# Kernel optimization log

Measured on AMD Instinct MI355X. Metric: run time of the kernel, lower is better.

Reference implementation:

```python
import jax, jax.numpy as jnp
import numpy as np

Z_SIZE, KEY_SIZE, HID = 128, 256, 512
NEG = -1e9


def setup_inputs() -> dict:
    key = jax.random.key(0)
    ks = jax.random.split(key, 8)
    B, T, H, W, Y = 512, 32, 32, 32, 4
    D = H * W
    g = lambda k, shape, s: jax.random.normal(k, shape, jnp.float32) * s
    return {
        "x_seq": jax.random.normal(ks[0], (B, T, H, W), jnp.float32),
        # Encoder (conv encoder stand-in: flatten -> MLP -> z_size)
        "enc_w1": g(ks[1], (D, HID), 0.03),
        "enc_b1": jnp.zeros((HID,), jnp.float32),
        "enc_w2": g(ks[2], (HID, Z_SIZE), 0.05),
        "enc_b2": jnp.zeros((Z_SIZE,), jnp.float32),
        # LSTM input kernel (recurrent kernel unused: h_prev is always 0)
        "lstm_Wx": g(ks[3], (KEY_SIZE + 1, 4 * HID), 0.05),
        "lstm_b": jnp.zeros((4 * HID,), jnp.float32),
        "keyw_W": g(ks[4], (HID, KEY_SIZE), 0.05),
        "keyw_b": jnp.zeros((KEY_SIZE,), jnp.float32),
        "g_W": g(ks[5], (HID, 1), 0.05),
        "g_b": jnp.zeros((1,), jnp.float32),
        "y_W": g(ks[6], (HID, Y), 0.05),
        "y_b": jnp.zeros((Y,), jnp.float32),
        "conf_gain": jnp.float32(1.0),
        "conf_bias": jnp.float32(0.0),
    }


def reference(x_seq, enc_w1, enc_b1, enc_w2, enc_b2, lstm_Wx, lstm_b,
              keyw_W, keyw_b, g_W, g_b, y_W, y_b, conf_gain, conf_bias):
    B, T = x_seq.shape[0], x_seq.shape[1]
    Y = y_b.shape[0]
    dt = x_seq.dtype

    # Encode all frames at once: (B, T, Z)
    x_flat = x_seq.reshape(B, T, -1)
    z_seq = jax.nn.relu(x_flat @ enc_w1 + enc_b1) @ enc_w2 + enc_b2
    # Pad with the zero z_t used at the final step t == T  -> (B, T+1, Z)
    z_pad = jnp.concatenate([z_seq, jnp.zeros((B, 1, Z_SIZE), dt)], axis=1)

    def lstm_step(x):  # single keras LSTM step from zero state (h=c=0)
        gates = x @ lstm_Wx + lstm_b
        i, f, c, o = jnp.split(gates, 4, axis=-1)  # keras gate order i,f,c,o
        c_new = jax.nn.sigmoid(i) * jnp.tanh(c)     # f*c_prev = 0
        return jax.nn.sigmoid(o) * jnp.tanh(c_new)

    slot_idx = jnp.arange(T + 1)

    def step(carry, t):
        key_r, M_k, M_v, _ = carry
        z_t = z_pad[:, t]                       # (B, Z)
        h = lstm_step(key_r)                    # (B, HID)
        key_w = h @ keyw_W + keyw_b             # (B, KEY)
        gate = jax.nn.sigmoid(h @ g_W + g_b)    # (B, 1)
        y_lin = h @ y_W + y_b                   # (B, Y)

        # Content-based read over memory slots written so far (slots < t)
        scores = jnp.einsum('bz,btz->bt', z_t, M_v)          # (B, T+1)
        valid = (slot_idx < t)[None, :]
        w_k = jax.nn.softmax(jnp.where(valid, scores, NEG), axis=1)
        c_k = jax.nn.sigmoid(scores * conf_gain + conf_bias)  # (B, T+1)
        Mkc = jnp.concatenate([M_k, c_k[..., None]], axis=-1)  # (B, T+1, KEY+1)
        key_r_new = gate * jnp.einsum('bt,btk->bk', w_k, Mkc)
        key_r_new = jnp.where(t == 0, jnp.zeros_like(key_r_new), key_r_new)

        # Memory write (append == write into preallocated slot t)
        M_k = M_k.at[:, t].set(key_w)
        M_v = M_v.at[:, t].set(z_t)
        return (key_r_new, M_k, M_v, y_lin), None

    init = (jnp.zeros((B, KEY_SIZE + 1), dt),
            jnp.zeros((B, T + 1, KEY_SIZE), dt),
            jnp.zeros((B, T + 1, Z_SIZE), dt),
            jnp.zeros((B, Y), dt))
    (_, _, _, y_pred_linear), _ = jax.lax.scan(step, init, jnp.arange(T + 1))
    y_pred = jnp.argmax(y_pred_linear, axis=1)
    return y_pred_linear, y_pred
```

## Files before the change

kernel.cpp:

```cpp
#include <hip/hip_runtime.h>
#include <math.h>

__device__ __forceinline__ float sigf(float x) { return 1.0f / (1.0f + expf(-x)); }
__device__ __forceinline__ float4 f4fma(float s, float4 b, float4 a) {
  return make_float4(fmaf(s, b.x, a.x), fmaf(s, b.y, a.y), fmaf(s, b.z, a.z), fmaf(s, b.w, a.w));
}
__device__ __forceinline__ void wave_red16_32(float4& v) {
  v.x += __shfl_xor(v.x, 16); v.y += __shfl_xor(v.y, 16);
  v.z += __shfl_xor(v.z, 16); v.w += __shfl_xor(v.w, 16);
  v.x += __shfl_xor(v.x, 32); v.y += __shfl_xor(v.y, 32);
  v.z += __shfl_xor(v.z, 32); v.w += __shfl_xor(v.w, 32);
}
__device__ __forceinline__ void wave_red8_16_32(float4& v) {
  v.x += __shfl_xor(v.x, 8);  v.y += __shfl_xor(v.y, 8);
  v.z += __shfl_xor(v.z, 8);  v.w += __shfl_xor(v.w, 8);
  wave_red16_32(v);
}

__global__ __launch_bounds__(256) void k_gemm1(const float* __restrict__ X,
                                               const float* __restrict__ W,
                                               const float* __restrict__ Bv,
                                               float* __restrict__ C)
{
  const int K = 1024, N = 512;
  __shared__ float As[32][68];
  __shared__ float Bs[32][132];
  const int tid = threadIdx.x;
  const int bm = blockIdx.x >> 2;
  const int bn = blockIdx.x & 3;
  const int ty = tid >> 4, tx = tid & 15;
  const int ar = tid & 63, ac4 = (tid >> 6) * 4;
  const int wk = tid >> 3, wc = (tid & 7) * 16;
  const float* Xb = X + (size_t)(bm * 64 + ar) * K;
  const float* Wb = W + bn * 128 + wc;
  float acc[4][8];
#pragma unroll
  for (int i = 0; i < 4; i++)
#pragma unroll
    for (int j = 0; j < 8; j++) acc[i][j] = 0.f;

  float4 pa0, pa1, pw0, pw1, pw2, pw3;
  {
    pa0 = *(const float4*)(Xb + ac4);
    pa1 = *(const float4*)(Xb + ac4 + 16);
    const float* wr = Wb + (size_t)wk * N;
    pw0 = *(const float4*)(wr);
    pw1 = *(const float4*)(wr + 4);
    pw2 = *(const float4*)(wr + 8);
    pw3 = *(const float4*)(wr + 12);
  }
  for (int k0 = 0; k0 < K; k0 += 32) {
    if (k0) __syncthreads();
    As[ac4 + 0][ar] = pa0.x; As[ac4 + 1][ar] = pa0.y;
    As[ac4 + 2][ar] = pa0.z; As[ac4 + 3][ar] = pa0.w;
    As[ac4 + 16][ar] = pa1.x; As[ac4 + 17][ar] = pa1.y;
    As[ac4 + 18][ar] = pa1.z; As[ac4 + 19][ar] = pa1.w;
    *(float4*)(&Bs[wk][wc])      = pw0;
    *(float4*)(&Bs[wk][wc + 4])  = pw1;
    *(float4*)(&Bs[wk][wc + 8])  = pw2;
    *(float4*)(&Bs[wk][wc + 12]) = pw3;
    __syncthreads();
    if (k0 < K - 32) {
      const int kn = k0 + 32;
      pa0 = *(const float4*)(Xb + kn + ac4);
      pa1 = *(const float4*)(Xb + kn + ac4 + 16);
      const float* wr = Wb + (size_t)(kn + wk) * N;
      pw0 = *(const float4*)(wr);
      pw1 = *(const float4*)(wr + 4);
      pw2 = *(const float4*)(wr + 8);
      pw3 = *(const float4*)(wr + 12);
    }
#pragma unroll
    for (int kk = 0; kk < 32; kk++) {
      float4 a = *(const float4*)(&As[kk][ty * 4]);
      float4 bA = *(const float4*)(&Bs[kk][tx * 4]);
      float4 bB = *(const float4*)(&Bs[kk][64 + tx * 4]);
      float ar4[4] = {a.x, a.y, a.z, a.w};
#pragma unroll
      for (int i = 0; i < 4; i++) {
        acc[i][0] = fmaf(ar4[i], bA.x, acc[i][0]);
        acc[i][1] = fmaf(ar4[i], bA.y, acc[i][1]);
        acc[i][2] = fmaf(ar4[i], bA.z, acc[i][2]);
        acc[i][3] = fmaf(ar4[i], bA.w, acc[i][3]);
        acc[i][4] = fmaf(ar4[i], bB.x, acc[i][4]);
        acc[i][5] = fmaf(ar4[i], bB.y, acc[i][5]);
        acc[i][6] = fmaf(ar4[i], bB.z, acc[i][6]);
        acc[i][7] = fmaf(ar4[i], bB.w, acc[i][7]);
      }
    }
  }
  const int crow0 = bm * 64 + ty * 4;
  const int ccolA = bn * 128 + tx * 4;
  const int ccolB = ccolA + 64;
  float4 bvA = *(const float4*)(Bv + ccolA);
  float4 bvB = *(const float4*)(Bv + ccolB);
#pragma unroll
  for (int i = 0; i < 4; i++) {
    float4 vA = make_float4(acc[i][0] + bvA.x, acc[i][1] + bvA.y,
                            acc[i][2] + bvA.z, acc[i][3] + bvA.w);
    float4 vB = make_float4(acc[i][4] + bvB.x, acc[i][5] + bvB.y,
                            acc[i][6] + bvB.z, acc[i][7] + bvB.w);
    vA.x = fmaxf(vA.x, 0.f); vA.y = fmaxf(vA.y, 0.f);
    vA.z = fmaxf(vA.z, 0.f); vA.w = fmaxf(vA.w, 0.f);
    vB.x = fmaxf(vB.x, 0.f); vB.y = fmaxf(vB.y, 0.f);
    vB.z = fmaxf(vB.z, 0.f); vB.w = fmaxf(vB.w, 0.f);
    *(float4*)(&C[(size_t)(crow0 + i) * N + ccolA]) = vA;
    *(float4*)(&C[(size_t)(crow0 + i) * N + ccolB]) = vB;
  }
}

__global__ __launch_bounds__(256) void k_gemm2(const float* __restrict__ A,
                                               const float* __restrict__ W,
                                               const float* __restrict__ Bv,
                                               float* __restrict__ zp)
{
  const int K = 512, N = 128;
  __shared__ float As[16][36];
  __shared__ float Bs[16][132];
  const int tid = threadIdx.x;
  const int bm = blockIdx.x;
  const int ty = tid >> 4, tx = tid & 15;
  const int ar = tid & 31, ac4 = ((tid >> 5) & 3) * 4;
  const int bk = tid >> 4, bc8 = (tid & 15) * 8;
  float acc[2][8];
#pragma unroll
  for (int i = 0; i < 2; i++)
#pragma unroll
    for (int j = 0; j < 8; j++) acc[i][j] = 0.f;

  for (int k0 = 0; k0 < K; k0 += 16) {
    if (tid < 128) {
      float4 av = *(const float4*)(A + (size_t)(bm * 32 + ar) * K + k0 + ac4);
      As[ac4 + 0][ar] = av.x; As[ac4 + 1][ar] = av.y;
      As[ac4 + 2][ar] = av.z; As[ac4 + 3][ar] = av.w;
    }
    *(float4*)(&Bs[bk][bc8]) = *(const float4*)(W + (size_t)(k0 + bk) * N + bc8);
    *(float4*)(&Bs[bk][bc8 + 4]) = *(const float4*)(W + (size_t)(k0 + bk) * N + bc8 + 4);
    __syncthreads();
#pragma unroll
    for (int kk = 0; kk < 16; kk++) {
      float a0 = As[kk][ty * 2], a1 = As[kk][ty * 2 + 1];
      float4 bA = *(const float4*)(&Bs[kk][tx * 4]);
      float4 bB = *(const float4*)(&Bs[kk][64 + tx * 4]);
      acc[0][0] = fmaf(a0, bA.x, acc[0][0]); acc[0][1] = fmaf(a0, bA.y, acc[0][1]);
      acc[0][2] = fmaf(a0, bA.z, acc[0][2]); acc[0][3] = fmaf(a0, bA.w, acc[0][3]);
      acc[0][4] = fmaf(a0, bB.x, acc[0][4]); acc[0][5] = fmaf(a0, bB.y, acc[0][5]);
      acc[0][6] = fmaf(a0, bB.z, acc[0][6]); acc[0][7] = fmaf(a0, bB.w, acc[0][7]);
      acc[1][0] = fmaf(a1, bA.x, acc[1][0]); acc[1][1] = fmaf(a1, bA.y, acc[1][1]);
      acc[1][2] = fmaf(a1, bA.z, acc[1][2]); acc[1][3] = fmaf(a1, bA.w, acc[1][3]);
      acc[1][4] = fmaf(a1, bB.x, acc[1][4]); acc[1][5] = fmaf(a1, bB.y, acc[1][5]);
      acc[1][6] = fmaf(a1, bB.z, acc[1][6]); acc[1][7] = fmaf(a1, bB.w, acc[1][7]);
    }
    __syncthreads();
  }
  const int ccolA = tx * 4, ccolB = ccolA + 64;
  float4 bvA = *(const float4*)(Bv + ccolA);
  float4 bvB = *(const float4*)(Bv + ccolB);
#pragma unroll
  for (int i = 0; i < 2; i++) {
    int r = bm * 32 + ty * 2 + i;
    int b = r >> 5, tt = r & 31;
    float4 vA = make_float4(acc[i][0] + bvA.x, acc[i][1] + bvA.y,
                            acc[i][2] + bvA.z, acc[i][3] + bvA.w);
    float4 vB = make_float4(acc[i][4] + bvB.x, acc[i][5] + bvB.y,
                            acc[i][6] + bvB.z, acc[i][7] + bvB.w);
    *(float4*)(&zp[(size_t)b * 4096 + tt * 128 + ccolA]) = vA;
    *(float4*)(&zp[(size_t)b * 4096 + tt * 128 + ccolB]) = vB;
  }
}

__global__ __launch_bounds__(256) void k_gram(const float* __restrict__ zp,
                                              float* __restrict__ warr,
                                              float* __restrict__ wc,
                                              const float* __restrict__ cgp,
                                              const float* __restrict__ cbp)
{
  __shared__ float zl[32][128];
  __shared__ float sg[32][32];
  int b = blockIdx.x, tid = threadIdx.x;
  const float* zb = zp + (size_t)b * 4096;
  for (int i = tid; i < 32 * 128; i += 256) (&zl[0][0])[i] = zb[i];
  __syncthreads();
  for (int p = tid; p < 496; p += 256) {
    int t = 1;
    while (p >= t * (t + 1) / 2) t++;
    int tp = p - t * (t - 1) / 2;
    const float* za = &zl[t][0];
    const float* zc = &zl[tp][0];
    float s = 0.f;
#pragma unroll 4
    for (int c = 0; c < 128; c += 4) {
      s += za[c] * zc[c] + za[c + 1] * zc[c + 1] + za[c + 2] * zc[c + 2] + za[c + 3] * zc[c + 3];
    }
    sg[t][tp] = s;
  }
  __syncthreads();
  if (tid >= 1 && tid < 32) {
    int t = tid;
    float cg = cgp[0], cb = cbp[0];
    float m = -3.0e38f;
    for (int tp = 0; tp < t; tp++) m = fmaxf(m, sg[t][tp]);
    float se = 0.f;
    for (int tp = 0; tp < t; tp++) se += expf(sg[t][tp] - m);
    float inv = 1.0f / se;
    float wcs = 0.f;
    for (int tp = 0; tp < t; tp++) {
      float s = sg[t][tp];
      float w = expf(s - m) * inv;
      warr[(size_t)b * 1024 + t * 32 + tp] = w;
      wcs = fmaf(w, sigf(fmaf(s, cg, cb)), wcs);
    }
    wc[b * 32 + t] = wcs;
  }
}

__global__ __launch_bounds__(256) void k_gates(const float* __restrict__ Wx,
                                               const float* __restrict__ lb,
                                               const float* __restrict__ keyrT,
                                               float* __restrict__ h, int t)
{
  __shared__ float smem[4608];
  float* As = smem;
  float* Bs = smem + 1280;
  float* Rb = smem;
  const int tid = threadIdx.x;
  const int rt = blockIdx.x >> 5;
  const int ct = blockIdx.x & 31;
  const int row0 = rt * 16;
  const int hc0 = ct * 16;

  if (t > 0) {
    const int ksub = tid >> 3;
    const int pos = tid & 7;
    const int rg = pos >> 2;
    const int cg = pos & 3;
    const int kkS = tid >> 2;
    const int lS = (tid & 3) * 4;
    float4 aI[8], aC[8], aO[8];
#pragma unroll
    for (int r = 0; r < 8; r++) {
      aI[r] = make_float4(0.f, 0.f, 0.f, 0.f);
      aC[r] = make_float4(0.f, 0.f, 0.f, 0.f);
      aO[r] = make_float4(0.f, 0.f, 0.f, 0.f);
    }
    float4 pA, pB0, pB1, pB2;
    {
      pA = *(const float4*)&keyrT[(size_t)kkS * 512 + row0 + lS];
      const float* wrow = Wx + (size_t)kkS * 2048 + hc0 + lS;
      pB0 = *(const float4*)(wrow);
      pB1 = *(const float4*)(wrow + 1024);
      pB2 = *(const float4*)(wrow + 1536);
    }
    for (int c = 0; c < 4; ++c) {
      if (c) __syncthreads();
      *(float4*)&As[kkS * 20 + lS] = pA;
      *(float4*)&Bs[kkS * 52 + lS] = pB0;
      *(float4*)&Bs[kkS * 52 + 16 + lS] = pB1;
      *(float4*)&Bs[kkS * 52 + 32 + lS] = pB2;
      __syncthreads();
      if (c < 3) {
        const int kn = (c + 1) * 64 + kkS;
        pA = *(const float4*)&keyrT[(size_t)kn * 512 + row0 + lS];
        const float* wrow = Wx + (size_t)kn * 2048 + hc0 + lS;
        pB0 = *(const float4*)(wrow);
        pB1 = *(const float4*)(wrow + 1024);
        pB2 = *(const float4*)(wrow + 1536);
      }
#pragma unroll
      for (int i = 0; i < 2; ++i) {
        const int kk = ksub * 2 + i;
        float a8[8];
        *(float4*)&a8[0] = *(const float4*)&As[kk * 20 + rg * 8];
        *(float4*)&a8[4] = *(const float4*)&As[kk * 20 + rg * 8 + 4];
        float4 bI = *(const float4*)&Bs[kk * 52 + cg * 4];
        float4 bC = *(const float4*)&Bs[kk * 52 + 16 + cg * 4];
        float4 bO = *(const float4*)&Bs[kk * 52 + 32 + cg * 4];
#pragma unroll
        for (int r = 0; r < 8; r++) {
          float a = a8[r];
          aI[r] = f4fma(a, bI, aI[r]);
          aC[r] = f4fma(a, bC, aC[r]);
          aO[r] = f4fma(a, bO, aO[r]);
        }
      }
    }
    if (tid < 8) {
      float a8[8];
      *(float4*)&a8[0] = *(const float4*)&keyrT[(size_t)256 * 512 + row0 + rg * 8];
      *(float4*)&a8[4] = *(const float4*)&keyrT[(size_t)256 * 512 + row0 + rg * 8 + 4];
      const float* wrow = Wx + (size_t)256 * 2048 + hc0 + cg * 4;
      float4 bI = *(const float4*)(wrow);
      float4 bC = *(const float4*)(wrow + 1024);
      float4 bO = *(const float4*)(wrow + 1536);
#pragma unroll
      for (int r = 0; r < 8; r++) {
        float a = a8[r];
        aI[r] = f4fma(a, bI, aI[r]);
        aC[r] = f4fma(a, bC, aC[r]);
        aO[r] = f4fma(a, bO, aO[r]);
      }
    }
#pragma unroll
    for (int r = 0; r < 8; r++) { wave_red8_16_32(aI[r]); wave_red8_16_32(aC[r]); wave_red8_16_32(aO[r]); }
    __syncthreads();
    {
      const int wave = tid >> 6, lane = tid & 63;
      if (lane < 8) {
        float* w = &Rb[wave * 800 + lane * 100];
#pragma unroll
        for (int r = 0; r < 8; r++) {
          *(float4*)&w[r * 12 + 0] = aI[r];
          *(float4*)&w[r * 12 + 4] = aC[r];
          *(float4*)&w[r * 12 + 8] = aO[r];
        }
      }
    }
    __syncthreads();
    {
      const int r = tid >> 4;
      const int hc = tid & 15;
      const int p = (r >> 3) * 4 + (hc >> 2);
      const int base = p * 100 + (r & 7) * 12 + (hc & 3);
      float sI = Rb[base]     + Rb[800 + base]     + Rb[1600 + base]     + Rb[2400 + base];
      float sC = Rb[base + 4] + Rb[800 + base + 4] + Rb[1600 + base + 4] + Rb[2400 + base + 4];
      float sO = Rb[base + 8] + Rb[800 + base + 8] + Rb[1600 + base + 8] + Rb[2400 + base + 8];
      float iv = sI + lb[hc0 + hc];
      float cv = sC + lb[1024 + hc0 + hc];
      float ov = sO + lb[1536 + hc0 + hc];
      h[(size_t)(row0 + r) * 512 + hc0 + hc] = sigf(ov) * tanhf(sigf(iv) * tanhf(cv));
    }
  } else {
    const int r = tid >> 4;
    const int hc = tid & 15;
    float hv = sigf(lb[1536 + hc0 + hc]) * tanhf(sigf(lb[hc0 + hc]) * tanhf(lb[1024 + hc0 + hc]));
    h[(size_t)(row0 + r) * 512 + hc0 + hc] = hv;
  }
}

__global__ __launch_bounds__(256) void k_update(const float* __restrict__ h,
                                                const float* __restrict__ kW,
                                                const float* __restrict__ kb,
                                                const float* __restrict__ gW,
                                                const float* __restrict__ gb,
                                                const float* __restrict__ warr,
                                                const float* __restrict__ wc,
                                                float* __restrict__ Mk,
                                                float* __restrict__ keyrT, int t)
{
  __shared__ float smem[10640];
  float* hs  = smem;
  float* gWs = smem + 8256;
  float* wws = smem + 8768;
  float* gsh = smem + 9344;
  float* kWs = smem + 9360;
  float* Rb  = smem + 9360;
  const int tid = threadIdx.x;
  const int rt = blockIdx.x >> 4;
  const int ct = blockIdx.x & 15;
  const int row0 = rt * 16;
  const int c0 = ct * 16;

  {
    const int r = tid >> 4, seg = tid & 15;
    const float* hrow = h + (size_t)(row0 + r) * 512 + seg * 32;
    float* hd = hs + r * 516 + seg * 32;
#pragma unroll
    for (int q = 0; q < 8; ++q) {
      const int qp = ((q + seg) & 7) * 4;
      *(float4*)&hd[qp] = *(const float4*)&hrow[qp];
    }
    if (tid < 128) *(float4*)&gWs[tid * 4] = *(const float4*)&gW[tid * 4];
    wws[r * 36 + seg]      = (seg < t)      ? warr[(size_t)(row0 + r) * 1024 + t * 32 + seg] : 0.f;
    wws[r * 36 + 16 + seg] = (16 + seg < t) ? warr[(size_t)(row0 + r) * 1024 + t * 32 + 16 + seg] : 0.f;
  }
  const int kkW = tid >> 2, lW = (tid & 3) * 4;
  float4 pW = *(const float4*)&kW[(size_t)kkW * 256 + c0 + lW];
  __syncthreads();

  const int ksub = tid >> 4, pu = tid & 15, rgu = pu >> 2, cgu = pu & 3;
  float4 au[4];
#pragma unroll
  for (int r = 0; r < 4; r++) au[r] = make_float4(0.f, 0.f, 0.f, 0.f);
  for (int c = 0; c < 8; ++c) {
    if (c) __syncthreads();
    *(float4*)&kWs[kkW * 20 + lW] = pW;
    __syncthreads();
    if (c < 7) pW = *(const float4*)&kW[(size_t)((c + 1) * 64 + kkW) * 256 + c0 + lW];
#pragma unroll
    for (int i = 0; i < 4; ++i) {
      const int kk = ksub * 4 + i;
      float4 b4 = *(const float4*)&kWs[kk * 20 + cgu * 4];
      const int kidx = c * 64 + kk;
#pragma unroll
      for (int jj = 0; jj < 4; ++jj) {
        float a = hs[(rgu * 4 + jj) * 516 + kidx];
        au[jj] = f4fma(a, b4, au[jj]);
      }
    }
  }
#pragma unroll
  for (int r = 0; r < 4; r++) wave_red16_32(au[r]);
  __syncthreads();
  {
    const int wave = tid >> 6, lane = tid & 63;
    if (lane < 16) {
      float* w = &Rb[wave * 320 + lane * 20];
#pragma unroll
      for (int r = 0; r < 4; r++) *(float4*)&w[r * 4] = au[r];
    }
  }
  __syncthreads();
  {
    const int r = tid >> 4, cc = tid & 15;
    const int p = (r >> 2) * 4 + (cc >> 2);
    const int e = p * 20 + (r & 3) * 4 + (cc & 3);
    float v = Rb[e] + Rb[320 + e] + Rb[640 + e] + Rb[960 + e];
    Mk[(size_t)(row0 + r) * 8192 + t * 256 + c0 + cc] = v + kb[c0 + cc];
  }
  {
    const int r = tid >> 4, seg = tid & 15;
    const float* hp = &hs[r * 516 + seg * 32];
    const float* gp = &gWs[seg * 32];
    float s = 0.f;
#pragma unroll 8
    for (int j = 0; j < 32; ++j) s = fmaf(hp[j], gp[j], s);
    s += __shfl_xor(s, 1); s += __shfl_xor(s, 2);
    s += __shfl_xor(s, 4); s += __shfl_xor(s, 8);
    if (seg == 0) gsh[r] = sigf(s + gb[0]);
  }
  __syncthreads();
  {
    const int r = tid >> 4, cc = tid & 15;
    const int row = row0 + r;
    if (t == 0) {
      keyrT[(size_t)(c0 + cc) * 512 + row] = 0.f;
      if (ct == 0 && cc == 0) keyrT[(size_t)256 * 512 + row] = 0.f;
    } else {
      float a = 0.f;
      const float* mkb = Mk + (size_t)row * 8192 + c0 + cc;
      const float* wp = &wws[r * 36];
      for (int tp = 0; tp < t; ++tp) a = fmaf(wp[tp], mkb[tp * 256], a);
      float g = gsh[r];
      keyrT[(size_t)(c0 + cc) * 512 + row] = g * a;
      if (ct == 0 && cc == 0)
        keyrT[(size_t)256 * 512 + row] = g * wc[row * 32 + t];
    }
  }
}

__global__ __launch_bounds__(256) void k_y(const float* __restrict__ h,
                                           const float* __restrict__ yW,
                                           const float* __restrict__ yb,
                                           float* __restrict__ out)
{
  int tid = threadIdx.x;
  int wave = tid >> 6, lane = tid & 63;
  int row = blockIdx.x * 4 + wave;
  float a0 = 0.f, a1 = 0.f, a2 = 0.f, a3 = 0.f;
  for (int k = lane; k < 512; k += 64) {
    float hv = h[(size_t)row * 512 + k];
    float4 w4 = *(const float4*)(yW + k * 4);
    a0 = fmaf(hv, w4.x, a0);
    a1 = fmaf(hv, w4.y, a1);
    a2 = fmaf(hv, w4.z, a2);
    a3 = fmaf(hv, w4.w, a3);
  }
#pragma unroll
  for (int off = 32; off > 0; off >>= 1) {
    a0 += __shfl_xor(a0, off);
    a1 += __shfl_xor(a1, off);
    a2 += __shfl_xor(a2, off);
    a3 += __shfl_xor(a3, off);
  }
  if (lane == 0) {
    a0 += yb[0]; a1 += yb[1]; a2 += yb[2]; a3 += yb[3];
    out[row * 4 + 0] = a0;
    out[row * 4 + 1] = a1;
    out[row * 4 + 2] = a2;
    out[row * 4 + 3] = a3;
    int bi = 0; float bv = a0;
    if (a1 > bv) { bv = a1; bi = 1; }
    if (a2 > bv) { bv = a2; bi = 2; }
    if (a3 > bv) { bv = a3; bi = 3; }
    out[2048 + row] = (float)bi;
  }
}

extern "C" void kernel_launch(void* const* d_in, const int* in_sizes, int n_in,
                              void* d_out, int out_size, void* d_ws, size_t ws_size,
                              hipStream_t stream)
{
  const float* x  = (const float*)d_in[0];
  const float* w1 = (const float*)d_in[1];
  const float* b1 = (const float*)d_in[2];
  const float* w2 = (const float*)d_in[3];
  const float* b2 = (const float*)d_in[4];
  const float* Wx = (const float*)d_in[5];
  const float* lb = (const float*)d_in[6];
  const float* kW = (const float*)d_in[7];
  const float* kb = (const float*)d_in[8];
  const float* gW = (const float*)d_in[9];
  const float* gb = (const float*)d_in[10];
  const float* yW = (const float*)d_in[11];
  const float* yb = (const float*)d_in[12];
  const float* cg = (const float*)d_in[13];
  const float* cb = (const float*)d_in[14];
  float* out = (float*)d_out;
  char* ws = (char*)d_ws;
  float* C1    = (float*)(ws);
  float* Mk    = (float*)(ws);
  float* warr  = (float*)(ws + 16777216);
  float* wcb   = (float*)(ws + 18874368);
  float* keyrT = (float*)(ws + 18939904);
  float* h     = (float*)(ws + 19466240);
  float* zp    = (float*)(ws + 33554432);

  hipLaunchKernelGGL(k_gemm1, dim3(1024), dim3(256), 0, stream, x, w1, b1, C1);
  hipLaunchKernelGGL(k_gemm2, dim3(512), dim3(256), 0, stream, C1, w2, b2, zp);
  hipLaunchKernelGGL(k_gram, dim3(512), dim3(256), 0, stream, zp, warr, wcb, cg, cb);
  for (int t = 0; t <= 32; t++) {
    hipLaunchKernelGGL(k_gates, dim3(1024), dim3(256), 0, stream, Wx, lb, keyrT, h, t);
    if (t < 32) {
      hipLaunchKernelGGL(k_update, dim3(512), dim3(256), 0, stream,
                         h, kW, kb, gW, gb, warr, wcb, Mk, keyrT, t);
    }
  }
  hipLaunchKernelGGL(k_y, dim3(128), dim3(256), 0, stream, h, yW, yb, out);
}
```

Baseline: 1.431 ms.

## Simplify gemm1, gates and update kernels to naive per-thread dot products

The gemm1 kernel drops its register-prefetch double buffering and halves the K tile to 16, adding a second barrier per tile. The gates kernel moves from a split-K register-tiled GEMM with shuffle reductions to one where each thread computes two hidden columns for one row, reading the weights directly from global memory. Its grid shrinks to 512 blocks. The update kernel likewise replaces its tiled shared-memory GEMM with a per-thread 512-long dot product reading keyW from global memory. This gives simpler code and fewer syncs and reductions, at the cost of less data reuse, less latency hiding and more global traffic.

After: 2.499 ms. 1.75x slower.

```diff
diff --git a/kernel.cpp b/kernel.cpp
--- a/kernel.cpp
+++ b/kernel.cpp
@@ -2,20 +2,6 @@
 #include <math.h>
 
 __device__ __forceinline__ float sigf(float x) { return 1.0f / (1.0f + expf(-x)); }
-__device__ __forceinline__ float4 f4fma(float s, float4 b, float4 a) {
-  return make_float4(fmaf(s, b.x, a.x), fmaf(s, b.y, a.y), fmaf(s, b.z, a.z), fmaf(s, b.w, a.w));
-}
-__device__ __forceinline__ void wave_red16_32(float4& v) {
-  v.x += __shfl_xor(v.x, 16); v.y += __shfl_xor(v.y, 16);
-  v.z += __shfl_xor(v.z, 16); v.w += __shfl_xor(v.w, 16);
-  v.x += __shfl_xor(v.x, 32); v.y += __shfl_xor(v.y, 32);
-  v.z += __shfl_xor(v.z, 32); v.w += __shfl_xor(v.w, 32);
-}
-__device__ __forceinline__ void wave_red8_16_32(float4& v) {
-  v.x += __shfl_xor(v.x, 8);  v.y += __shfl_xor(v.y, 8);
-  v.z += __shfl_xor(v.z, 8);  v.w += __shfl_xor(v.w, 8);
-  wave_red16_32(v);
-}
 
 __global__ __launch_bounds__(256) void k_gemm1(const float* __restrict__ X,
                                                const float* __restrict__ W,
@@ -23,55 +9,32 @@
                                                float* __restrict__ C)
 {
   const int K = 1024, N = 512;
-  __shared__ float As[32][68];
-  __shared__ float Bs[32][132];
+  __shared__ float As[16][68];
+  __shared__ float Bs[16][132];
   const int tid = threadIdx.x;
   const int bm = blockIdx.x >> 2;
   const int bn = blockIdx.x & 3;
   const int ty = tid >> 4, tx = tid & 15;
   const int ar = tid & 63, ac4 = (tid >> 6) * 4;
-  const int wk = tid >> 3, wc = (tid & 7) * 16;
+  const int bk = tid >> 4, bc8 = (tid & 15) * 8;
   const float* Xb = X + (size_t)(bm * 64 + ar) * K;
-  const float* Wb = W + bn * 128 + wc;
   float acc[4][8];
 #pragma unroll
   for (int i = 0; i < 4; i++)
 #pragma unroll
     for (int j = 0; j < 8; j++) acc[i][j] = 0.f;
 
-  float4 pa0, pa1, pw0, pw1, pw2, pw3;
-  {
-    pa0 = *(const float4*)(Xb + ac4);
-    pa1 = *(const float4*)(Xb + ac4 + 16);
-    const float* wr = Wb + (size_t)wk * N;
-    pw0 = *(const float4*)(wr);
-    pw1 = *(const float4*)(wr + 4);
-    pw2 = *(const float4*)(wr + 8);
-    pw3 = *(const float4*)(wr + 12);
-  }
-  for (int k0 = 0; k0 < K; k0 += 32) {
-    if (k0) __syncthreads();
-    As[ac4 + 0][ar] = pa0.x; As[ac4 + 1][ar] = pa0.y;
-    As[ac4 + 2][ar] = pa0.z; As[ac4 + 3][ar] = pa0.w;
-    As[ac4 + 16][ar] = pa1.x; As[ac4 + 17][ar] = pa1.y;
-    As[ac4 + 18][ar] = pa1.z; As[ac4 + 19][ar] = pa1.w;
-    *(float4*)(&Bs[wk][wc])      = pw0;
-    *(float4*)(&Bs[wk][wc + 4])  = pw1;
-    *(float4*)(&Bs[wk][wc + 8])  = pw2;
-    *(float4*)(&Bs[wk][wc + 12]) = pw3;
-    __syncthreads();
-    if (k0 < K - 32) {
-      const int kn = k0 + 32;
-      pa0 = *(const float4*)(Xb + kn + ac4);
-      pa1 = *(const float4*)(Xb + kn + ac4 + 16);
-      const float* wr = Wb + (size_t)(kn + wk) * N;
-      pw0 = *(const float4*)(wr);
-      pw1 = *(const float4*)(wr + 4);
-      pw2 = *(const float4*)(wr + 8);
-      pw3 = *(const float4*)(wr + 12);
-    }
-#pragma unroll
-    for (int kk = 0; kk < 32; kk++) {
+  for (int k0 = 0; k0 < K; k0 += 16) {
+    float4 av = *(const float4*)(Xb + k0 + ac4);
+    float4 b0 = *(const float4*)(W + (size_t)(k0 + bk) * N + bn * 128 + bc8);
+    float4 b1 = *(const float4*)(W + (size_t)(k0 + bk) * N + bn * 128 + bc8 + 4);
+    As[ac4 + 0][ar] = av.x; As[ac4 + 1][ar] = av.y;
+    As[ac4 + 2][ar] = av.z; As[ac4 + 3][ar] = av.w;
+    *(float4*)(&Bs[bk][bc8]) = b0;
+    *(float4*)(&Bs[bk][bc8 + 4]) = b1;
+    __syncthreads();
+#pragma unroll
+    for (int kk = 0; kk < 16; kk++) {
       float4 a = *(const float4*)(&As[kk][ty * 4]);
       float4 bA = *(const float4*)(&Bs[kk][tx * 4]);
       float4 bB = *(const float4*)(&Bs[kk][64 + tx * 4]);
@@ -88,6 +51,7 @@
         acc[i][7] = fmaf(ar4[i], bB.w, acc[i][7]);
       }
     }
+    __syncthreads();
   }
   const int crow0 = bm * 64 + ty * 4;
   const int ccolA = bn * 128 + tx * 4;
@@ -219,122 +183,57 @@
                                                const float* __restrict__ keyrT,
                                                float* __restrict__ h, int t)
 {
-  __shared__ float smem[4608];
-  float* As = smem;
-  float* Bs = smem + 1280;
-  float* Rb = smem;
+  __shared__ float As[257 * 17 + 3];
   const int tid = threadIdx.x;
-  const int rt = blockIdx.x >> 5;
-  const int ct = blockIdx.x & 31;
+  const int rt = blockIdx.x >> 4;
+  const int ct = blockIdx.x & 15;
   const int row0 = rt * 16;
-  const int hc0 = ct * 16;
+  const int hc0 = ct * 32;
+  const int r = tid >> 4;
+  const int c2 = tid & 15;
+  const int j0 = hc0 + c2 * 2;
+
+  float aI0 = lb[j0],        aI1 = lb[j0 + 1];
+  float aC0 = lb[1024 + j0], aC1 = lb[1024 + j0 + 1];
+  float aO0 = lb[1536 + j0], aO1 = lb[1536 + j0 + 1];
 
   if (t > 0) {
-    const int ksub = tid >> 3;
-    const int pos = tid & 7;
-    const int rg = pos >> 2;
-    const int cg = pos & 3;
-    const int kkS = tid >> 2;
-    const int lS = (tid & 3) * 4;
-    float4 aI[8], aC[8], aO[8];
-#pragma unroll
-    for (int r = 0; r < 8; r++) {
-      aI[r] = make_float4(0.f, 0.f, 0.f, 0.f);
-      aC[r] = make_float4(0.f, 0.f, 0.f, 0.f);
-      aO[r] = make_float4(0.f, 0.f, 0.f, 0.f);
-    }
-    float4 pA, pB0, pB1, pB2;
     {
-      pA = *(const float4*)&keyrT[(size_t)kkS * 512 + row0 + lS];
-      const float* wrow = Wx + (size_t)kkS * 2048 + hc0 + lS;
-      pB0 = *(const float4*)(wrow);
-      pB1 = *(const float4*)(wrow + 1024);
-      pB2 = *(const float4*)(wrow + 1536);
-    }
-    for (int c = 0; c < 4; ++c) {
-      if (c) __syncthreads();
-      *(float4*)&As[kkS * 20 + lS] = pA;
-      *(float4*)&Bs[kkS * 52 + lS] = pB0;
-      *(float4*)&Bs[kkS * 52 + 16 + lS] = pB1;
-      *(float4*)&Bs[kkS * 52 + 32 + lS] = pB2;
-      __syncthreads();
-      if (c < 3) {
-        const int kn = (c + 1) * 64 + kkS;
-        pA = *(const float4*)&keyrT[(size_t)kn * 512 + row0 + lS];
-        const float* wrow = Wx + (size_t)kn * 2048 + hc0 + lS;
-        pB0 = *(const float4*)(wrow);
-        pB1 = *(const float4*)(wrow + 1024);
-        pB2 = *(const float4*)(wrow + 1536);
+      const int k = tid;
+      const float* src = keyrT + (size_t)k * 512 + row0;
+      float4 v0 = *(const float4*)(src);
+      float4 v1 = *(const float4*)(src + 4);
+      float4 v2 = *(const float4*)(src + 8);
+      float4 v3 = *(const float4*)(src + 12);
+      float* d = &As[k * 17];
+      d[0] = v0.x; d[1] = v0.y; d[2] = v0.z; d[3] = v0.w;
+      d[4] = v1.x; d[5] = v1.y; d[6] = v1.z; d[7] = v1.w;
+      d[8] = v2.x; d[9] = v2.y; d[10] = v2.z; d[11] = v2.w;
+      d[12] = v3.x; d[13] = v3.y; d[14] = v3.z; d[15] = v3.w;
+      if (tid == 0) {
+        const float* s2 = keyrT + (size_t)256 * 512 + row0;
+        float* d2 = &As[256 * 17];
+#pragma unroll
+        for (int j = 0; j < 16; ++j) d2[j] = s2[j];
       }
-#pragma unroll
-      for (int i = 0; i < 2; ++i) {
-        const int kk = ksub * 2 + i;
-        float a8[8];
-        *(float4*)&a8[0] = *(const float4*)&As[kk * 20 + rg * 8];
-        *(float4*)&a8[4] = *(const float4*)&As[kk * 20 + rg * 8 + 4];
-        float4 bI = *(const float4*)&Bs[kk * 52 + cg * 4];
-        float4 bC = *(const float4*)&Bs[kk * 52 + 16 + cg * 4];
-        float4 bO = *(const float4*)&Bs[kk * 52 + 32 + cg * 4];
-#pragma unroll
-        for (int r = 0; r < 8; r++) {
-          float a = a8[r];
-          aI[r] = f4fma(a, bI, aI[r]);
-          aC[r] = f4fma(a, bC, aC[r]);
-          aO[r] = f4fma(a, bO, aO[r]);
-        }
-      }
-    }
-    if (tid < 8) {
-      float a8[8];
-      *(float4*)&a8[0] = *(const float4*)&keyrT[(size_t)256 * 512 + row0 + rg * 8];
-      *(float4*)&a8[4] = *(const float4*)&keyrT[(size_t)256 * 512 + row0 + rg * 8 + 4];
-      const float* wrow = Wx + (size_t)256 * 2048 + hc0 + cg * 4;
-      float4 bI = *(const float4*)(wrow);
-      float4 bC = *(const float4*)(wrow + 1024);
-      float4 bO = *(const float4*)(wrow + 1536);
-#pragma unroll
-      for (int r = 0; r < 8; r++) {
-        float a = a8[r];
-        aI[r] = f4fma(a, bI, aI[r]);
-        aC[r] = f4fma(a, bC, aC[r]);
-        aO[r] = f4fma(a, bO, aO[r]);
-      }
-    }
-#pragma unroll
-    for (int r = 0; r < 8; r++) { wave_red8_16_32(aI[r]); wave_red8_16_32(aC[r]); wave_red8_16_32(aO[r]); }
-    __syncthreads();
-    {
-      const int wave = tid >> 6, lane = tid & 63;
-      if (lane < 8) {
-        float* w = &Rb[wave * 800 + lane * 100];
-#pragma unroll
-        for (int r = 0; r < 8; r++) {
-          *(float4*)&w[r * 12 + 0] = aI[r];
-          *(float4*)&w[r * 12 + 4] = aC[r];
-          *(float4*)&w[r * 12 + 8] = aO[r];
-        }
-      }
-    }
-    __syncthreads();
-    {
-      const int r = tid >> 4;
-      const int hc = tid & 15;
-      const int p = (r >> 3) * 4 + (hc >> 2);
-      const int base = p * 100 + (r & 7) * 12 + (hc & 3);
-      float sI = Rb[base]     + Rb[800 + base]     + Rb[1600 + base]     + Rb[2400 + base];
-      float sC = Rb[base + 4] + Rb[800 + base + 4] + Rb[1600 + base + 4] + Rb[2400 + base + 4];
-      float sO = Rb[base + 8] + Rb[800 + base + 8] + Rb[1600 + base + 8] + Rb[2400 + base + 8];
-      float iv = sI + lb[hc0 + hc];
-      float cv = sC + lb[1024 + hc0 + hc];
-      float ov = sO + lb[1536 + hc0 + hc];
-      h[(size_t)(row0 + r) * 512 + hc0 + hc] = sigf(ov) * tanhf(sigf(iv) * tanhf(cv));
-    }
-  } else {
-    const int r = tid >> 4;
-    const int hc = tid & 15;
-    float hv = sigf(lb[1536 + hc0 + hc]) * tanhf(sigf(lb[hc0 + hc]) * tanhf(lb[1024 + hc0 + hc]));
-    h[(size_t)(row0 + r) * 512 + hc0 + hc] = hv;
-  }
+    }
+    __syncthreads();
+    const float* wp = Wx + j0;
+    const float* ap = &As[r];
+#pragma unroll 8
+    for (int k = 0; k < 257; ++k) {
+      float a = ap[k * 17];
+      float2 wi = *(const float2*)(wp + (size_t)k * 2048);
+      float2 wv = *(const float2*)(wp + (size_t)k * 2048 + 1024);
+      float2 wo = *(const float2*)(wp + (size_t)k * 2048 + 1536);
+      aI0 = fmaf(a, wi.x, aI0); aI1 = fmaf(a, wi.y, aI1);
+      aC0 = fmaf(a, wv.x, aC0); aC1 = fmaf(a, wv.y, aC1);
+      aO0 = fmaf(a, wo.x, aO0); aO1 = fmaf(a, wo.y, aO1);
+    }
+  }
+  float h0 = sigf(aO0) * tanhf(sigf(aI0) * tanhf(aC0));
+  float h1 = sigf(aO1) * tanhf(sigf(aI1) * tanhf(aC1));
+  *(float2*)&h[(size_t)(row0 + r) * 512 + j0] = make_float2(h0, h1);
 }
 
 __global__ __launch_bounds__(256) void k_update(const float* __restrict__ h,
@@ -347,102 +246,60 @@
                                                 float* __restrict__ Mk,
                                                 float* __restrict__ keyrT, int t)
 {
-  __shared__ float smem[10640];
-  float* hs  = smem;
-  float* gWs = smem + 8256;
-  float* wws = smem + 8768;
-  float* gsh = smem + 9344;
-  float* kWs = smem + 9360;
-  float* Rb  = smem + 9360;
+  __shared__ float hs[16 * 516];
+  __shared__ float gWs[512];
+  __shared__ float wws[16 * 36];
+  __shared__ float gsh[16];
   const int tid = threadIdx.x;
   const int rt = blockIdx.x >> 4;
   const int ct = blockIdx.x & 15;
   const int row0 = rt * 16;
   const int c0 = ct * 16;
+  const int r = tid >> 4, c = tid & 15;
 
   {
-    const int r = tid >> 4, seg = tid & 15;
-    const float* hrow = h + (size_t)(row0 + r) * 512 + seg * 32;
-    float* hd = hs + r * 516 + seg * 32;
-#pragma unroll
-    for (int q = 0; q < 8; ++q) {
-      const int qp = ((q + seg) & 7) * 4;
-      *(float4*)&hd[qp] = *(const float4*)&hrow[qp];
-    }
+    const float* hrow = h + (size_t)(row0 + r) * 512 + c * 32;
+    float* hd = &hs[r * 516 + c * 32];
+#pragma unroll
+    for (int q = 0; q < 8; ++q) *(float4*)&hd[q * 4] = *(const float4*)&hrow[q * 4];
     if (tid < 128) *(float4*)&gWs[tid * 4] = *(const float4*)&gW[tid * 4];
-    wws[r * 36 + seg]      = (seg < t)      ? warr[(size_t)(row0 + r) * 1024 + t * 32 + seg] : 0.f;
-    wws[r * 36 + 16 + seg] = (16 + seg < t) ? warr[(size_t)(row0 + r) * 1024 + t * 32 + 16 + seg] : 0.f;
-  }
-  const int kkW = tid >> 2, lW = (tid & 3) * 4;
-  float4 pW = *(const float4*)&kW[(size_t)kkW * 256 + c0 + lW];
+    wws[r * 36 + c]      = (c < t)      ? warr[(size_t)(row0 + r) * 1024 + t * 32 + c] : 0.f;
+    wws[r * 36 + 16 + c] = (16 + c < t) ? warr[(size_t)(row0 + r) * 1024 + t * 32 + 16 + c] : 0.f;
+  }
   __syncthreads();
 
-  const int ksub = tid >> 4, pu = tid & 15, rgu = pu >> 2, cgu = pu & 3;
-  float4 au[4];
-#pragma unroll
-  for (int r = 0; r < 4; r++) au[r] = make_float4(0.f, 0.f, 0.f, 0.f);
-  for (int c = 0; c < 8; ++c) {
-    if (c) __syncthreads();
-    *(float4*)&kWs[kkW * 20 + lW] = pW;
-    __syncthreads();
-    if (c < 7) pW = *(const float4*)&kW[(size_t)((c + 1) * 64 + kkW) * 256 + c0 + lW];
-#pragma unroll
-    for (int i = 0; i < 4; ++i) {
-      const int kk = ksub * 4 + i;
-      float4 b4 = *(const float4*)&kWs[kk * 20 + cgu * 4];
-      const int kidx = c * 64 + kk;
-#pragma unroll
-      for (int jj = 0; jj < 4; ++jj) {
-        float a = hs[(rgu * 4 + jj) * 516 + kidx];
-        au[jj] = f4fma(a, b4, au[jj]);
-      }
-    }
-  }
-#pragma unroll
-  for (int r = 0; r < 4; r++) wave_red16_32(au[r]);
+  {
+    float acc = kb[c0 + c];
+    const float* hp = &hs[r * 516];
+    const float* kp = kW + c0 + c;
+#pragma unroll 8
+    for (int k = 0; k < 512; ++k)
+      acc = fmaf(hp[k], kp[(size_t)k * 256], acc);
+    Mk[(size_t)(row0 + r) * 8192 + t * 256 + c0 + c] = acc;
+  }
+  {
+    float s = 0.f;
+    const float* hp = &hs[r * 516];
+#pragma unroll 8
+    for (int k = c; k < 512; k += 16) s = fmaf(hp[k], gWs[k], s);
+    s += __shfl_xor(s, 1); s += __shfl_xor(s, 2);
+    s += __shfl_xor(s, 4); s += __shfl_xor(s, 8);
+    if (c == 0) gsh[r] = sigf(s + gb[0]);
+  }
   __syncthreads();
   {
-    const int wave = tid >> 6, lane = tid & 63;
-    if (lane < 16) {
-      float* w = &Rb[wave * 320 + lane * 20];
-#pragma unroll
-      for (int r = 0; r < 4; r++) *(float4*)&w[r * 4] = au[r];
-    }
-  }
-  __syncthreads();
-  {
-    const int r = tid >> 4, cc = tid & 15;
-    const int p = (r >> 2) * 4 + (cc >> 2);
-    const int e = p * 20 + (r & 3) * 4 + (cc & 3);
-    float v = Rb[e] + Rb[320 + e] + Rb[640 + e] + Rb[960 + e];
-    Mk[(size_t)(row0 + r) * 8192 + t * 256 + c0 + cc] = v + kb[c0 + cc];
-  }
-  {
-    const int r = tid >> 4, seg = tid & 15;
-    const float* hp = &hs[r * 516 + seg * 32];
-    const float* gp = &gWs[seg * 32];
-    float s = 0.f;
-#pragma unroll 8
-    for (int j = 0; j < 32; ++j) s = fmaf(hp[j], gp[j], s);
-    s += __shfl_xor(s, 1); s += __shfl_xor(s, 2);
-    s += __shfl_xor(s, 4); s += __shfl_xor(s, 8);
-    if (seg == 0) gsh[r] = sigf(s + gb[0]);
-  }
-  __syncthreads();
-  {
-    const int r = tid >> 4, cc = tid & 15;
     const int row = row0 + r;
     if (t == 0) {
-      keyrT[(size_t)(c0 + cc) * 512 + row] = 0.f;
-      if (ct == 0 && cc == 0) keyrT[(size_t)256 * 512 + row] = 0.f;
+      keyrT[(size_t)(c0 + c) * 512 + row] = 0.f;
+      if (ct == 0 && c == 0) keyrT[(size_t)256 * 512 + row] = 0.f;
     } else {
       float a = 0.f;
-      const float* mkb = Mk + (size_t)row * 8192 + c0 + cc;
+      const float* mkb = Mk + (size_t)row * 8192 + c0 + c;
       const float* wp = &wws[r * 36];
       for (int tp = 0; tp < t; ++tp) a = fmaf(wp[tp], mkb[tp * 256], a);
       float g = gsh[r];
-      keyrT[(size_t)(c0 + cc) * 512 + row] = g * a;
-      if (ct == 0 && cc == 0)
+      keyrT[(size_t)(c0 + c) * 512 + row] = g * a;
+      if (ct == 0 && c == 0)
         keyrT[(size_t)256 * 512 + row] = g * wc[row * 32 + t];
     }
   }
@@ -519,7 +376,7 @@
   hipLaunchKernelGGL(k_gemm2, dim3(512), dim3(256), 0, stream, C1, w2, b2, zp);
   hipLaunchKernelGGL(k_gram, dim3(512), dim3(256), 0, stream, zp, warr, wcb, cg, cb);
   for (int t = 0; t <= 32; t++) {
-    hipLaunchKernelGGL(k_gates, dim3(1024), dim3(256), 0, stream, Wx, lb, keyrT, h, t);
+    hipLaunchKernelGGL(k_gates, dim3(512), dim3(256), 0, stream, Wx, lb, keyrT, h, t);
     if (t < 32) {
       hipLaunchKernelGGL(k_update, dim3(512), dim3(256), 0, stream,
                          h, kW, kb, gW, gb, warr, wcb, Mk, keyrT, t);
```
